# Kernel tuning notes

Hardware: AMD Instinct MI355X
Metric: run time of the kernel (lower is better)

## Reference

```python
import jax, jax.numpy as jnp
import numpy as np

B = 16384      # batch
N = 128        # number of DNPU nodes (experts)
I = 3          # data electrodes per node
C = 4          # control electrodes per node
E = I + C      # total electrodes = 7
H = 90         # surrogate-model hidden width
L = 3          # number of extra hidden layers


def setup_inputs() -> dict:
    key = jax.random.key(0)
    ks = jax.random.split(key, 8)
    s_in = 1.0 / np.sqrt(E)
    s_h = 1.0 / np.sqrt(H)
    return {
        "x": jax.random.normal(ks[0], (B, N * I), dtype=jnp.float32),
        "controls": jax.random.uniform(ks[1], (N, C), dtype=jnp.float32, minval=-1.2, maxval=0.6),
        "W_in": jax.random.normal(ks[2], (N, E, H), dtype=jnp.float32) * s_in,
        "b_in": jax.random.normal(ks[3], (N, H), dtype=jnp.float32) * 0.1,
        "W_hid": jax.random.normal(ks[4], (L, N, H, H), dtype=jnp.float32) * s_h,
        "b_hid": jax.random.normal(ks[5], (L, N, H), dtype=jnp.float32) * 0.1,
        "W_out": jax.random.normal(ks[6], (N, H), dtype=jnp.float32) * s_h,
        "b_out": jax.random.normal(ks[7], (N,), dtype=jnp.float32) * 0.1,
    }


def reference(x, controls, W_in, b_in, W_hid, b_hid, W_out, b_out):
    # DNPU_Layer: partition x into N chunks of I, each node merges its data
    # electrodes with its learned control voltages into a 7-electrode vector,
    # evaluates the shared surrogate MLP with per-node parameters, outputs 1
    # current per node; results are concatenated along dim 1 -> [B, N].
    b = x.shape[0]
    xd = x.reshape(b, N, I)                                   # partition_input
    ctrl = jnp.broadcast_to(controls[None], (b, N, C))        # per-node controls
    e = jnp.concatenate([xd, ctrl], axis=-1)                  # [B, N, E]
    h = jax.nn.relu(jnp.einsum('bne,neh->bnh', e, W_in) + b_in)
    for l in range(L):  # fixed small layer count
        h = jax.nn.relu(jnp.einsum('bnh,nhk->bnk', h, W_hid[l]) + b_hid[l])
    out = jnp.einsum('bnh,nh->bn', h, W_out) + b_out          # [B, N]
    return out
```

## Files before the change

### kernel.cpp

```cpp
#include <hip/hip_runtime.h>
#include <stdint.h>

namespace {
constexpr int kB  = 16384;
constexpr int kN  = 128;
constexpr int kI  = 3;
constexpr int kC  = 4;
constexpr int kH  = 90;
constexpr int kL  = 3;
constexpr int BT  = 64;
constexpr int KP  = 96;
constexpr int TILE_USH = 18 * 512;
constexpr size_t WT_BYTES = (size_t)4 * kN * TILE_USH * 2;
constexpr size_t WO_OFF   = WT_BYTES;
constexpr size_t XK_OFF   = WO_OFF + (size_t)kN * KP * 4;
constexpr size_t OT_OFF   = XK_OFF + (size_t)kN * kI * kB * 2;
}

typedef __attribute__((ext_vector_type(8))) short bf16x8;
typedef __attribute__((ext_vector_type(4))) float f32x4;

__device__ __forceinline__ uint32_t pack_bf16(float lo, float hi) {
#if __has_builtin(__builtin_amdgcn_cvt_pk_bf16_f32)
  auto r = __builtin_amdgcn_cvt_pk_bf16_f32(lo, hi);
  union { decltype(r) v; uint32_t u; } c; c.v = r; return c.u;
#else
  union { float f; uint32_t i; } a, b; a.f = lo; b.f = hi;
  uint32_t ua = a.i + 0x8000u;
  uint32_t ub = b.i + 0x8000u;
  return __builtin_amdgcn_perm(ub, ua, 0x07060302);
#endif
}
__device__ __forceinline__ ushort f2bf(float f) {
  union { float f; uint32_t i; } v; v.f = f;
  uint32_t u = v.i + 0x7FFFu + ((v.i >> 16) & 1u);
  return (ushort)(u >> 16);
}

__global__ __launch_bounds__(256) void prep_kernel(
    const float* __restrict__ x,
    const float* __restrict__ W_in, const float* __restrict__ b_in,
    const float* __restrict__ W_hid, const float* __restrict__ b_hid,
    const float* __restrict__ W_out, const float* __restrict__ b_out,
    ushort* __restrict__ wt, float* __restrict__ wo, ushort* __restrict__ xk)
{
  __shared__ float smem[kH * (kH + 1) + kH];
  const int tid = threadIdx.x;
  const int bid = blockIdx.x;

  if (bid < 4 * kN) {
    float* ldsw = smem;
    float* ldsb = smem + kH * (kH + 1);
    const int node  = bid & (kN - 1);
    const int layer = bid >> 7;
    const int ksrc  = (layer == 0) ? (kI + kC) : kH;
    const float* src;
    const float* bsrc;
    if (layer == 0) { src = W_in + (size_t)node * (kI + kC) * kH; bsrc = b_in + (size_t)node * kH; }
    else {
      int l = layer - 1;
      src  = W_hid + (size_t)(l * kN + node) * kH * kH;
      bsrc = b_hid + (size_t)(l * kN + node) * kH;
    }
    for (int idx = tid; idx < ksrc * kH; idx += 256)
      ldsw[(idx / kH) * (kH + 1) + (idx % kH)] = src[idx];
    if (tid < kH) ldsb[tid] = bsrc[tid];
    __syncthreads();
    ushort* dst = wt + (size_t)bid * TILE_USH;
    const int nush = (layer == 0) ? 6 * 512 : TILE_USH;
    for (int idx = tid; idx < nush; idx += 256) {
      int fb = idx >> 9, lane = (idx >> 3) & 63, i = idx & 7;
      int mt = fb % 6, ks = fb / 6;
      int j = mt * 16 + (lane & 15);
      int k = ks * 32 + (lane >> 4) * 8 + i;
      float v = 0.f;
      if (j < kH) {
        if (k < ksrc)       v = ldsw[k * (kH + 1) + j];
        else if (k == ksrc) v = ldsb[j];
      }
      dst[idx] = f2bf(v);
    }
  } else if (bid < 4 * kN + 4) {
    int base = (bid - 4 * kN) * 3072;
    for (int t = 0; t < 12; ++t) {
      int idx = base + t * 256 + tid;
      int node = idx / KP, j = idx % KP;
      float v = 0.f;
      if (j < kH)       v = W_out[node * kH + j];
      else if (j == kH) v = b_out[node];
      wo[idx] = v;
    }
  } else {
    int xb = bid - (4 * kN + 4);
    int b0 = (xb & 255) * 64;
    int c0 = (xb >> 8) * 96;
    float* lds = smem;
    for (int idx = tid; idx < 64 * 96; idx += 256) {
      int r = idx / 96, c = idx % 96;
      lds[r * 97 + c] = x[(size_t)(b0 + r) * (kN * kI) + c0 + c];
    }
    __syncthreads();
    for (int idx = tid; idx < 96 * 64; idx += 256) {
      int nk = idx >> 6, b = idx & 63;
      xk[(size_t)(c0 + nk) * kB + b0 + b] = f2bf(lds[b * 97 + nk]);
    }
  }
}

__global__ __launch_bounds__(64, 3) void dnpu_kernel(
    const ushort* __restrict__ xk, const float* __restrict__ controls,
    const ushort* __restrict__ wt, const float* __restrict__ wo,
    float* __restrict__ outT)
{
  __shared__ __align__(16) ushort fbuf[12][BT][8];

  const int lane = threadIdx.x;
  const int node = (int)(blockIdx.x >> 8);
  const int m0   = (int)(blockIdx.x & 255) * BT;
  const int quad = lane >> 4;
  const int l16  = lane & 15;

  const f32x4 zf = (f32x4){0.f, 0.f, 0.f, 0.f};
  f32x4 acc[6][4];

  bf16x8 bfr0[4];
  {
    const ushort cb0 = f2bf(controls[node * kC + 0]);
    const ushort cb1 = f2bf(controls[node * kC + 1]);
    const ushort cb2 = f2bf(controls[node * kC + 2]);
    const ushort cb3 = f2bf(controls[node * kC + 3]);
    if (quad == 0) {
      const ushort* x0p = xk + (size_t)(node * kI + 0) * kB + m0 + l16;
      const ushort* x1p = xk + (size_t)(node * kI + 1) * kB + m0 + l16;
      const ushort* x2p = xk + (size_t)(node * kI + 2) * kB + m0 + l16;
#pragma unroll
      for (int nt = 0; nt < 4; ++nt) {
        union { ushort s[8]; bf16x8 v; } f;
        f.s[0] = x0p[nt * 16]; f.s[1] = x1p[nt * 16]; f.s[2] = x2p[nt * 16];
        f.s[3] = cb0; f.s[4] = cb1; f.s[5] = cb2; f.s[6] = cb3;
        f.s[7] = 0x3F80;
        bfr0[nt] = f.v;
      }
    } else {
#pragma unroll
      for (int nt = 0; nt < 4; ++nt)
        bfr0[nt] = (bf16x8){0,0,0,0,0,0,0,0};
    }
  }

  {
    const ushort* tl = wt + (size_t)(0 * kN + node) * TILE_USH;
#pragma unroll
    for (int mt = 0; mt < 6; ++mt) {
      bf16x8 afr = *(const bf16x8*)&tl[(size_t)mt * 512 + lane * 8];
#pragma unroll
      for (int nt = 0; nt < 4; ++nt)
        acc[mt][nt] = __builtin_amdgcn_mfma_f32_16x16x32_bf16(afr, bfr0[nt], zf, 0, 0, 0);
    }
  }

  auto write_h = [&]() {
#pragma unroll
    for (int mt = 0; mt < 6; ++mt) {
      const int kb = 2 * mt + (quad >> 1);
      const int i0 = (quad & 1) * 4;
#pragma unroll
      for (int nt = 0; nt < 4; ++nt) {
        float v0 = fmaxf(acc[mt][nt][0], 0.f);
        float v1 = fmaxf(acc[mt][nt][1], 0.f);
        float v2 = fmaxf(acc[mt][nt][2], 0.f);
        float v3 = fmaxf(acc[mt][nt][3], 0.f);
        if (mt == 5 && quad == 2) v2 = 1.0f;
        uint2 p;
        p.x = pack_bf16(v0, v1);
        p.y = pack_bf16(v2, v3);
        *(uint2*)&fbuf[kb][nt * 16 + l16][i0] = p;
      }
    }
  };

#pragma unroll
  for (int l = 0; l < kL; ++l) {
    const ushort* tl = wt + (size_t)((l + 1) * kN + node) * TILE_USH;
    write_h();

    {
      bf16x8 bfr[4];
#pragma unroll
      for (int nt = 0; nt < 4; ++nt)
        bfr[nt] = *(const bf16x8*)&fbuf[quad][nt * 16 + l16][0];
#pragma unroll
      for (int mt = 0; mt < 6; ++mt) {
        bf16x8 afr = *(const bf16x8*)&tl[(size_t)mt * 512 + lane * 8];
#pragma unroll
        for (int nt = 0; nt < 4; ++nt)
          acc[mt][nt] = __builtin_amdgcn_mfma_f32_16x16x32_bf16(afr, bfr[nt], zf, 0, 0, 0);
      }
    }
#pragma unroll
    for (int ks = 1; ks < 3; ++ks) {
      bf16x8 bfr[4];
#pragma unroll
      for (int nt = 0; nt < 4; ++nt)
        bfr[nt] = *(const bf16x8*)&fbuf[ks * 4 + quad][nt * 16 + l16][0];
#pragma unroll
      for (int mt = 0; mt < 6; ++mt) {
        bf16x8 afr = *(const bf16x8*)&tl[(size_t)(ks * 6 + mt) * 512 + lane * 8];
#pragma unroll
        for (int nt = 0; nt < 4; ++nt)
          acc[mt][nt] = __builtin_amdgcn_mfma_f32_16x16x32_bf16(afr, bfr[nt], acc[mt][nt], 0, 0, 0);
      }
    }
  }

  {
    float s[4] = {0.f, 0.f, 0.f, 0.f};
#pragma unroll
    for (int mt = 0; mt < 6; ++mt) {
      float4 wof = *(const float4*)&wo[node * KP + mt * 16 + quad * 4];
#pragma unroll
      for (int nt = 0; nt < 4; ++nt) {
        float h0 = fmaxf(acc[mt][nt][0], 0.f);
        float h1 = fmaxf(acc[mt][nt][1], 0.f);
        float h2 = fmaxf(acc[mt][nt][2], 0.f);
        float h3 = fmaxf(acc[mt][nt][3], 0.f);
        if (mt == 5 && quad == 2) h2 = 1.0f;
        s[nt] += h0 * wof.x + h1 * wof.y + h2 * wof.z + h3 * wof.w;
      }
    }
#pragma unroll
    for (int nt = 0; nt < 4; ++nt) {
      s[nt] += __shfl_xor(s[nt], 16);
      s[nt] += __shfl_xor(s[nt], 32);
    }
    float r = (quad == 0) ? s[0] : (quad == 1) ? s[1] : (quad == 2) ? s[2] : s[3];
    outT[(size_t)node * kB + m0 + lane] = r;
  }
}

__global__ __launch_bounds__(256) void transpose_out(
    const float* __restrict__ ot, float* __restrict__ out)
{
  __shared__ float t[64][65];
  const int b0 = (int)(blockIdx.x & 255) * 64;
  const int n0 = (int)(blockIdx.x >> 8) * 64;
  const int c  = threadIdx.x & 63;
  const int r4 = threadIdx.x >> 6;
#pragma unroll
  for (int i = 0; i < 16; ++i) {
    int n = r4 + i * 4;
    t[n][c] = ot[(size_t)(n0 + n) * kB + b0 + c];
  }
  __syncthreads();
#pragma unroll
  for (int i = 0; i < 16; ++i) {
    int b = r4 + i * 4;
    out[(size_t)(b0 + b) * kN + n0 + c] = t[c][b];
  }
}

extern "C" void kernel_launch(void* const* d_in, const int* in_sizes, int n_in,
                              void* d_out, int out_size, void* d_ws, size_t ws_size,
                              hipStream_t stream) {
  const float* x        = (const float*)d_in[0];
  const float* controls = (const float*)d_in[1];
  const float* W_in     = (const float*)d_in[2];
  const float* b_in     = (const float*)d_in[3];
  const float* W_hid    = (const float*)d_in[4];
  const float* b_hid    = (const float*)d_in[5];
  const float* W_out    = (const float*)d_in[6];
  const float* b_out    = (const float*)d_in[7];
  float* out = (float*)d_out;

  ushort* wt = (ushort*)d_ws;
  float*  wo = (float*)((char*)d_ws + WO_OFF);
  ushort* xk = (ushort*)((char*)d_ws + XK_OFF);
  float*  ot = (float*)((char*)d_ws + OT_OFF);

  hipLaunchKernelGGL(prep_kernel, dim3(4 * kN + 4 + 1024), dim3(256), 0, stream,
                     x, W_in, b_in, W_hid, b_hid, W_out, b_out, wt, wo, xk);

  dim3 grid(kN * (kB / BT));
  hipLaunchKernelGGL(dnpu_kernel, grid, dim3(BT), 0, stream,
                     xk, controls, wt, wo, ot);

  hipLaunchKernelGGL(transpose_out, dim3(512), dim3(256), 0, stream, ot, out);
}
```

Baseline: 246.7 us.

## Halve batch tile per wave and vectorize bf16 stores in prep kernel

Each wave in the main MLP kernel now processes 32 batch rows instead of 64, using two 16-column MFMA tiles instead of four. This halves the accumulator registers and the fbuf LDS footprint, and the launch-bounds hint is raised to four waves, aiming for more resident waves and more blocks. In exchange every weight fragment is reloaded twice as often per batch row, which raises global/L2 weight traffic. The prep kernel also builds 8 bf16 values per thread and writes them with 16-byte stores instead of scalar ushort stores.

```diff
diff --git a/kernel.cpp b/kernel.cpp
--- a/kernel.cpp
+++ b/kernel.cpp
@@ -8,7 +8,8 @@
 constexpr int kC  = 4;
 constexpr int kH  = 90;
 constexpr int kL  = 3;
-constexpr int BT  = 64;
+constexpr int BT  = 32;
+constexpr int NT  = 2;
 constexpr int KP  = 96;
 constexpr int TILE_USH = 18 * 512;
 constexpr size_t WT_BYTES = (size_t)4 * kN * TILE_USH * 2;
@@ -67,18 +68,31 @@
     if (tid < kH) ldsb[tid] = bsrc[tid];
     __syncthreads();
     ushort* dst = wt + (size_t)bid * TILE_USH;
-    const int nush = (layer == 0) ? 6 * 512 : TILE_USH;
-    for (int idx = tid; idx < nush; idx += 256) {
-      int fb = idx >> 9, lane = (idx >> 3) & 63, i = idx & 7;
-      int mt = fb % 6, ks = fb / 6;
-      int j = mt * 16 + (lane & 15);
-      int k = ks * 32 + (lane >> 4) * 8 + i;
-      float v = 0.f;
-      if (j < kH) {
-        if (k < ksrc)       v = ldsw[k * (kH + 1) + j];
-        else if (k == ksrc) v = ldsb[j];
-      }
-      dst[idx] = f2bf(v);
+    const int nch = (layer == 0) ? 384 : 1152;
+#pragma unroll
+    for (int it = 0; it < 5; ++it) {
+      int c = tid + it * 256;
+      if (c < nch) {
+        int fb = c >> 6, lane = c & 63;
+        int mt = fb % 6, ks = fb / 6;
+        int j = mt * 16 + (lane & 15);
+        int kb = ks * 32 + (lane >> 4) * 8;
+        float v[8];
+#pragma unroll
+        for (int i = 0; i < 8; ++i) {
+          int k = kb + i;
+          float t = 0.f;
+          if (j < kH) {
+            if (k < ksrc)       t = ldsw[k * (kH + 1) + j];
+            else if (k == ksrc) t = ldsb[j];
+          }
+          v[i] = t;
+        }
+        uint4 p;
+        p.x = pack_bf16(v[0], v[1]); p.y = pack_bf16(v[2], v[3]);
+        p.z = pack_bf16(v[4], v[5]); p.w = pack_bf16(v[6], v[7]);
+        *(uint4*)&dst[(size_t)c * 8] = p;
+      }
     }
   } else if (bid < 4 * kN + 4) {
     int base = (bid - 4 * kN) * 3072;
@@ -100,14 +114,22 @@
       lds[r * 97 + c] = x[(size_t)(b0 + r) * (kN * kI) + c0 + c];
     }
     __syncthreads();
-    for (int idx = tid; idx < 96 * 64; idx += 256) {
-      int nk = idx >> 6, b = idx & 63;
-      xk[(size_t)(c0 + nk) * kB + b0 + b] = f2bf(lds[b * 97 + nk]);
-    }
-  }
-}
-
-__global__ __launch_bounds__(64, 3) void dnpu_kernel(
+#pragma unroll
+    for (int it = 0; it < 3; ++it) {
+      int c = tid + it * 256;
+      int nk = c >> 3, b = (c & 7) * 8;
+      float v[8];
+#pragma unroll
+      for (int i = 0; i < 8; ++i) v[i] = lds[(b + i) * 97 + nk];
+      uint4 p;
+      p.x = pack_bf16(v[0], v[1]); p.y = pack_bf16(v[2], v[3]);
+      p.z = pack_bf16(v[4], v[5]); p.w = pack_bf16(v[6], v[7]);
+      *(uint4*)&xk[(size_t)(c0 + nk) * kB + b0 + b] = p;
+    }
+  }
+}
+
+__global__ __launch_bounds__(64, 4) void dnpu_kernel(
     const ushort* __restrict__ xk, const float* __restrict__ controls,
     const ushort* __restrict__ wt, const float* __restrict__ wo,
     float* __restrict__ outT)
@@ -115,15 +137,15 @@
   __shared__ __align__(16) ushort fbuf[12][BT][8];
 
   const int lane = threadIdx.x;
-  const int node = (int)(blockIdx.x >> 8);
-  const int m0   = (int)(blockIdx.x & 255) * BT;
+  const int node = (int)(blockIdx.x >> 9);
+  const int m0   = (int)(blockIdx.x & 511) * BT;
   const int quad = lane >> 4;
   const int l16  = lane & 15;
 
   const f32x4 zf = (f32x4){0.f, 0.f, 0.f, 0.f};
-  f32x4 acc[6][4];
-
-  bf16x8 bfr0[4];
+  f32x4 acc[6][NT];
+
+  bf16x8 bfr0[NT];
   {
     const ushort cb0 = f2bf(controls[node * kC + 0]);
     const ushort cb1 = f2bf(controls[node * kC + 1]);
@@ -134,7 +156,7 @@
       const ushort* x1p = xk + (size_t)(node * kI + 1) * kB + m0 + l16;
       const ushort* x2p = xk + (size_t)(node * kI + 2) * kB + m0 + l16;
 #pragma unroll
-      for (int nt = 0; nt < 4; ++nt) {
+      for (int nt = 0; nt < NT; ++nt) {
         union { ushort s[8]; bf16x8 v; } f;
         f.s[0] = x0p[nt * 16]; f.s[1] = x1p[nt * 16]; f.s[2] = x2p[nt * 16];
         f.s[3] = cb0; f.s[4] = cb1; f.s[5] = cb2; f.s[6] = cb3;
@@ -143,7 +165,7 @@
       }
     } else {
 #pragma unroll
-      for (int nt = 0; nt < 4; ++nt)
+      for (int nt = 0; nt < NT; ++nt)
         bfr0[nt] = (bf16x8){0,0,0,0,0,0,0,0};
     }
   }
@@ -154,7 +176,7 @@
     for (int mt = 0; mt < 6; ++mt) {
       bf16x8 afr = *(const bf16x8*)&tl[(size_t)mt * 512 + lane * 8];
 #pragma unroll
-      for (int nt = 0; nt < 4; ++nt)
+      for (int nt = 0; nt < NT; ++nt)
         acc[mt][nt] = __builtin_amdgcn_mfma_f32_16x16x32_bf16(afr, bfr0[nt], zf, 0, 0, 0);
     }
   }
@@ -165,7 +187,7 @@
       const int kb = 2 * mt + (quad >> 1);
       const int i0 = (quad & 1) * 4;
 #pragma unroll
-      for (int nt = 0; nt < 4; ++nt) {
+      for (int nt = 0; nt < NT; ++nt) {
         float v0 = fmaxf(acc[mt][nt][0], 0.f);
         float v1 = fmaxf(acc[mt][nt][1], 0.f);
         float v2 = fmaxf(acc[mt][nt][2], 0.f);
@@ -185,41 +207,41 @@
     write_h();
 
     {
-      bf16x8 bfr[4];
-#pragma unroll
-      for (int nt = 0; nt < 4; ++nt)
+      bf16x8 bfr[NT];
+#pragma unroll
+      for (int nt = 0; nt < NT; ++nt)
         bfr[nt] = *(const bf16x8*)&fbuf[quad][nt * 16 + l16][0];
 #pragma unroll
       for (int mt = 0; mt < 6; ++mt) {
         bf16x8 afr = *(const bf16x8*)&tl[(size_t)mt * 512 + lane * 8];
 #pragma unroll
-        for (int nt = 0; nt < 4; ++nt)
+        for (int nt = 0; nt < NT; ++nt)
           acc[mt][nt] = __builtin_amdgcn_mfma_f32_16x16x32_bf16(afr, bfr[nt], zf, 0, 0, 0);
       }
     }
 #pragma unroll
     for (int ks = 1; ks < 3; ++ks) {
-      bf16x8 bfr[4];
-#pragma unroll
-      for (int nt = 0; nt < 4; ++nt)
+      bf16x8 bfr[NT];
+#pragma unroll
+      for (int nt = 0; nt < NT; ++nt)
         bfr[nt] = *(const bf16x8*)&fbuf[ks * 4 + quad][nt * 16 + l16][0];
 #pragma unroll
       for (int mt = 0; mt < 6; ++mt) {
         bf16x8 afr = *(const bf16x8*)&tl[(size_t)(ks * 6 + mt) * 512 + lane * 8];
 #pragma unroll
-        for (int nt = 0; nt < 4; ++nt)
+        for (int nt = 0; nt < NT; ++nt)
           acc[mt][nt] = __builtin_amdgcn_mfma_f32_16x16x32_bf16(afr, bfr[nt], acc[mt][nt], 0, 0, 0);
       }
     }
   }
 
   {
-    float s[4] = {0.f, 0.f, 0.f, 0.f};
+    float s[NT] = {0.f, 0.f};
 #pragma unroll
     for (int mt = 0; mt < 6; ++mt) {
       float4 wof = *(const float4*)&wo[node * KP + mt * 16 + quad * 4];
 #pragma unroll
-      for (int nt = 0; nt < 4; ++nt) {
+      for (int nt = 0; nt < NT; ++nt) {
         float h0 = fmaxf(acc[mt][nt][0], 0.f);
         float h1 = fmaxf(acc[mt][nt][1], 0.f);
         float h2 = fmaxf(acc[mt][nt][2], 0.f);
@@ -229,12 +251,14 @@
       }
     }
 #pragma unroll
-    for (int nt = 0; nt < 4; ++nt) {
+    for (int nt = 0; nt < NT; ++nt) {
       s[nt] += __shfl_xor(s[nt], 16);
       s[nt] += __shfl_xor(s[nt], 32);
     }
-    float r = (quad == 0) ? s[0] : (quad == 1) ? s[1] : (quad == 2) ? s[2] : s[3];
-    outT[(size_t)node * kB + m0 + lane] = r;
+    if (quad < NT) {
+      float r = (quad == 0) ? s[0] : s[1];
+      outT[(size_t)node * kB + m0 + quad * 16 + l16] = r;
+    }
   }
 }
 
@@ -281,7 +305,7 @@
                      x, W_in, b_in, W_hid, b_hid, W_out, b_out, wt, wo, xk);
 
   dim3 grid(kN * (kB / BT));
-  hipLaunchKernelGGL(dnpu_kernel, grid, dim3(BT), 0, stream,
+  hipLaunchKernelGGL(dnpu_kernel, grid, dim3(64), 0, stream,
                      xk, controls, wt, wo, ot);
 
   hipLaunchKernelGGL(transpose_out, dim3(512), dim3(256), 0, stream, ot, out);
```

New measurement: 258.0 us. 1.05x slower.
